# Kernel tuning notes

Measured on AMD Instinct MI355X. Metric: run time of the kernel, lower is better.

## Reference

```python
import jax, jax.numpy as jnp
import numpy as np

B, CQ, CK, H, W = 8, 256, 256, 96, 96
EPS = 1e-4
SLOPE = 0.01  # torch LeakyReLU default


def conv1x1(x, w, b):
    # x: [B,Ci,H,W], w: [Co,Ci], b: [Co]
    return jnp.einsum('oi,bihw->bohw', w, x) + b[None, :, None, None]


def setup_inputs() -> dict:
    key = jax.random.key(0)
    ks = jax.random.split(key, 8)
    s = 0.02  # weight init scale for numerical sanity
    return {
        'q': jax.random.normal(ks[0], (B, CQ, H, W), jnp.float32),
        'v': jax.random.normal(ks[1], (B, CK, H, W), jnp.float32),
        'Wq': jax.random.normal(ks[2], (CQ, CQ), jnp.float32) * s,
        'bq': jnp.zeros((CQ,), jnp.float32),
        'Wk': jax.random.normal(ks[3], (CK, CK), jnp.float32) * s,
        'bk': jnp.zeros((CK,), jnp.float32),
        'Wv': jax.random.normal(ks[4], (CK, CQ), jnp.float32) * s,
        'bv': jnp.zeros((CK,), jnp.float32),
        'bn_gamma': jnp.ones((CQ,), jnp.float32),
        'bn_beta': jnp.zeros((CQ,), jnp.float32),
        'bn_mean': jnp.zeros((CQ,), jnp.float32),
        'bn_var': jnp.ones((CQ,), jnp.float32),
        'Wo1': jax.random.normal(ks[5], (CQ, CQ), jnp.float32) * s,
        'bo1': jnp.zeros((CQ,), jnp.float32),
        'Wo2': jax.random.normal(ks[6], (CQ, CQ), jnp.float32) * s,
        'bo2': jnp.zeros((CQ,), jnp.float32),
    }


def reference(q, v, Wq, bq, Wk, bk, Wv, bv, bn_gamma, bn_beta, bn_mean, bn_var, Wo1, bo1, Wo2, bo2):
    N = H * W
    query = conv1x1(q, Wq, bq).reshape(B, CQ, N)   # [B,CQ,N]
    key_t = conv1x1(v, Wk, bk).reshape(B, CK, N)   # [B,CK,N]
    value = conv1x1(q, Wv, bv).reshape(B, CK, N)   # [B,CK,N]
    # channel-attention: scores over channels, spatial is the contraction axis
    scale = float(N) ** 0.5
    scores = jnp.einsum('bcn,bdn->bcd', query, key_t) / scale  # [B,CQ,CK]
    attn = jax.nn.softmax(scores, axis=-1)
    out = jnp.einsum('bcd,bdn->bcn', attn, value)  # [B,CQ,N]
    # faithful permute(0,2,1).contiguous().view(B,-1,H,W): raw reshape of [B,N,CQ]
    out = jnp.transpose(out, (0, 2, 1)).reshape(B, CQ, H, W)
    # conv_out: BN (inference) -> LeakyReLU -> 1x1 conv -> LeakyReLU -> 1x1 conv
    inv = jax.lax.rsqrt(bn_var + EPS)
    out = (out - bn_mean[None, :, None, None]) * (bn_gamma * inv)[None, :, None, None] + bn_beta[None, :, None, None]
    out = jnp.where(out >= 0, out, SLOPE * out)
    out = conv1x1(out, Wo1, bo1)
    out = jnp.where(out >= 0, out, SLOPE * out)
    out = conv1x1(out, Wo2, bo2)
    return out
```

## Files before the change

### kernel.cpp

```cpp
#include <hip/hip_runtime.h>
#include <hip/hip_bf16.h>
#include <stdint.h>

#define CH     256
#define NSP    9216
#define NBATCH 8
#define NSPLIT 8
#define KSEG   1152

typedef unsigned short ushort_t;
using f32x4  = __attribute__((ext_vector_type(4))) float;
using bf16x8 = __attribute__((ext_vector_type(8))) short;

__device__ __forceinline__ ushort_t f2b(float f) {
  union { float f; uint32_t u; } v; v.f = f;
  return (ushort_t)((v.u + 0x7FFFu + ((v.u >> 16) & 1u)) >> 16);
}

__device__ __forceinline__ uint32_t swz(uint32_t row, uint32_t byte) {
  return row * 128u + (byte ^ ((row & 7u) << 4));
}

typedef __attribute__((address_space(3))) void       lds_void;
typedef const __attribute__((address_space(1))) void g_void;
__device__ __forceinline__ void glds16(const void* g, void* l) {
  __builtin_amdgcn_global_load_lds((g_void*)g, (lds_void*)l, 16, 0, 0);
}

__global__ void wconv_kernel(const float* __restrict__ w0, const float* __restrict__ w1,
                             const float* __restrict__ w2, const float* __restrict__ w3,
                             const float* __restrict__ w4, ushort_t* __restrict__ dst) {
  int gid = blockIdx.x * 256 + threadIdx.x;
  int m   = gid >> 13;
  int u   = gid & 8191;
  const float* W = (m == 0) ? w0 : (m == 1) ? w1 : (m == 2) ? w2 : (m == 3) ? w3 : w4;
  int lin = u * 16;
  int kc  = lin >> 15;
  int co  = (lin >> 7) & 255;
  int bb0 = lin & 127;
  int k0  = kc * 64 + ((bb0 ^ ((co & 7) << 4)) >> 1);
  const float* srow = W + co * 256 + k0;
  float4 a = *reinterpret_cast<const float4*>(srow);
  float4 c = *reinterpret_cast<const float4*>(srow + 4);
  ushort_t o[8] = {f2b(a.x), f2b(a.y), f2b(a.z), f2b(a.w),
                   f2b(c.x), f2b(c.y), f2b(c.z), f2b(c.w)};
  uint4 pk;
  pk.x = (uint32_t)o[0] | ((uint32_t)o[1] << 16);
  pk.y = (uint32_t)o[2] | ((uint32_t)o[3] << 16);
  pk.z = (uint32_t)o[4] | ((uint32_t)o[5] << 16);
  pk.w = (uint32_t)o[6] | ((uint32_t)o[7] << 16);
  *reinterpret_cast<uint4*>(dst + m * 65536 + (lin >> 1)) = pk;
}

template<int NOUT>
__global__ __launch_bounds__(256)
void proj_kernel(const ushort_t* __restrict__ Asw0, const float* __restrict__ bias0,
                 ushort_t* __restrict__ dst0,
                 const ushort_t* __restrict__ Asw1, const float* __restrict__ bias1,
                 char* __restrict__ valt,
                 const float* __restrict__ src) {
  const int b    = blockIdx.y;
  const int n0   = blockIdx.x * 64;
  const int tid  = threadIdx.x;
  const int lane = tid & 63;
  const int w    = tid >> 6;

  __shared__ __align__(16) unsigned char sA0[32768];
  __shared__ __align__(16) unsigned char sA1[(NOUT == 2) ? 32768 : 16];
  __shared__ __align__(16) unsigned char sB[8192];

  f32x4 acc0[4][4];
  f32x4 acc1[4][4];
  #pragma unroll
  for (int i = 0; i < 4; ++i)
    #pragma unroll
    for (int j = 0; j < 4; ++j)
      #pragma unroll
      for (int r = 0; r < 4; ++r) { acc0[i][j][r] = 0.f; acc1[i][j][r] = 0.f; }

  for (int kc = 0; kc < 4; ++kc) {
    const int k0 = kc * 64;
    if (kc > 0) __syncthreads();
    #pragma unroll
    for (int it = 0; it < 8; ++it) {
      int seg = (it * 4 + w) * 1024;
      glds16((const char*)Asw0 + kc * 32768 + seg + lane * 16,
             (void*)(sA0 + seg));
      if constexpr (NOUT == 2)
        glds16((const char*)Asw1 + kc * 32768 + seg + lane * 16,
               (void*)(sA1 + seg));
    }
    {
      const int ci0 = (tid >> 4) * 4;
      const int n4  = (tid & 15) * 4;
      float xv[4][4];
      #pragma unroll
      for (int r = 0; r < 4; ++r) {
        float4 t4 = *reinterpret_cast<const float4*>(
            src + ((size_t)b * CH + (k0 + ci0 + r)) * NSP + n0 + n4);
        xv[r][0] = t4.x; xv[r][1] = t4.y; xv[r][2] = t4.z; xv[r][3] = t4.w;
      }
      #pragma unroll
      for (int j = 0; j < 4; ++j) {
        uint64_t pk = (uint64_t)f2b(xv[0][j])
                    | ((uint64_t)f2b(xv[1][j]) << 16)
                    | ((uint64_t)f2b(xv[2][j]) << 32)
                    | ((uint64_t)f2b(xv[3][j]) << 48);
        *reinterpret_cast<uint64_t*>(&sB[swz(n4 + j, ci0 * 2)]) = pk;
      }
    }
    __syncthreads();
    #pragma unroll
    for (int ks = 0; ks < 2; ++ks) {
      const int kb = ks * 64 + (lane >> 4) * 16;
      bf16x8 fb[4], fa0[4];
      #pragma unroll
      for (int ni = 0; ni < 4; ++ni)
        fb[ni] = *reinterpret_cast<const bf16x8*>(&sB[swz(ni * 16 + (lane & 15), kb)]);
      #pragma unroll
      for (int mi = 0; mi < 4; ++mi)
        fa0[mi] = *reinterpret_cast<const bf16x8*>(&sA0[swz(w * 64 + mi * 16 + (lane & 15), kb)]);
      #pragma unroll
      for (int mi = 0; mi < 4; ++mi)
        #pragma unroll
        for (int ni = 0; ni < 4; ++ni)
          acc0[mi][ni] = __builtin_amdgcn_mfma_f32_16x16x32_bf16(fa0[mi], fb[ni], acc0[mi][ni], 0, 0, 0);
      if constexpr (NOUT == 2) {
        bf16x8 fa1[4];
        #pragma unroll
        for (int mi = 0; mi < 4; ++mi)
          fa1[mi] = *reinterpret_cast<const bf16x8*>(&sA1[swz(w * 64 + mi * 16 + (lane & 15), kb)]);
        #pragma unroll
        for (int mi = 0; mi < 4; ++mi)
          #pragma unroll
          for (int ni = 0; ni < 4; ++ni)
            acc1[mi][ni] = __builtin_amdgcn_mfma_f32_16x16x32_bf16(fa1[mi], fb[ni], acc1[mi][ni], 0, 0, 0);
      }
    }
  }
  #pragma unroll
  for (int mi = 0; mi < 4; ++mi) {
    const int coB = w * 64 + mi * 16 + ((lane >> 4) << 2);
    #pragma unroll
    for (int ni = 0; ni < 4; ++ni) {
      const int n = n0 + ni * 16 + (lane & 15);
      #pragma unroll
      for (int r = 0; r < 4; ++r) {
        const int co = coB + r;
        dst0[((size_t)b * CH + co) * NSP + n] = f2b(acc0[mi][ni][r] + bias0[co]);
      }
    }
  }
  if constexpr (NOUT == 2) {
    __syncthreads();
    #pragma unroll
    for (int mi = 0; mi < 4; ++mi) {
      const int co0 = w * 64 + mi * 16 + ((lane >> 4) << 2);
      #pragma unroll
      for (int ni = 0; ni < 4; ++ni) {
        const int nl = ni * 16 + (lane & 15);
        uint64_t pk = (uint64_t)f2b(acc1[mi][ni][0] + bias1[co0])
                    | ((uint64_t)f2b(acc1[mi][ni][1] + bias1[co0 + 1]) << 16)
                    | ((uint64_t)f2b(acc1[mi][ni][2] + bias1[co0 + 2]) << 32)
                    | ((uint64_t)f2b(acc1[mi][ni][3] + bias1[co0 + 3]) << 48);
        *reinterpret_cast<uint64_t*>(&sA0[nl * 512 + ((co0 * 2) ^ ((nl & 7) << 4))]) = pk;
      }
    }
    __syncthreads();
    char* vb = valt + (size_t)b * (NSP * 512) + (size_t)n0 * 512;
    #pragma unroll
    for (int i = 0; i < 8; ++i) {
      *reinterpret_cast<uint4*>(vb + tid * 128 + i * 16) =
          *reinterpret_cast<const uint4*>(sA0 + tid * 128 + i * 16);
    }
  }
}

__global__ __launch_bounds__(256)
void scores_kernel(const ushort_t* __restrict__ qry, const ushort_t* __restrict__ key,
                   float* __restrict__ part) {
  const int b  = blockIdx.z;
  const int s  = blockIdx.y;
  const int c0 = (blockIdx.x >> 1) * 128;
  const int d0 = (blockIdx.x & 1) * 128;
  const int tid  = threadIdx.x;
  const int lane = tid & 63;
  const int wm = (tid >> 7) & 1;
  const int wn = (tid >> 6) & 1;

  __shared__ __align__(16) unsigned char sQ[128 * 128];
  __shared__ __align__(16) unsigned char sK[128 * 128];

  f32x4 acc[4][4];
  #pragma unroll
  for (int i = 0; i < 4; ++i)
    #pragma unroll
    for (int j = 0; j < 4; ++j)
      #pragma unroll
      for (int r = 0; r < 4; ++r) acc[i][j][r] = 0.f;

  for (int kc = 0; kc < KSEG / 64; ++kc) {
    const int k0 = s * KSEG + kc * 64;
    #pragma unroll
    for (int it = 0; it < 4; ++it) {
      int slot = it * 256 + tid;
      int row  = slot >> 3;
      int seg  = slot & 7;
      *reinterpret_cast<uint4*>(&sQ[swz(row, seg * 16)]) =
          *reinterpret_cast<const uint4*>(qry + ((size_t)b * CH + c0 + row) * NSP + k0 + seg * 8);
      *reinterpret_cast<uint4*>(&sK[swz(row, seg * 16)]) =
          *reinterpret_cast<const uint4*>(key + ((size_t)b * CH + d0 + row) * NSP + k0 + seg * 8);
    }
    __syncthreads();
    #pragma unroll
    for (int ks = 0; ks < 2; ++ks) {
      const int kb = ks * 64 + (lane >> 4) * 16;
      bf16x8 fq[4], fk[4];
      #pragma unroll
      for (int mi = 0; mi < 4; ++mi)
        fq[mi] = *reinterpret_cast<const bf16x8*>(&sQ[swz(wm * 64 + mi * 16 + (lane & 15), kb)]);
      #pragma unroll
      for (int ni = 0; ni < 4; ++ni)
        fk[ni] = *reinterpret_cast<const bf16x8*>(&sK[swz(wn * 64 + ni * 16 + (lane & 15), kb)]);
      #pragma unroll
      for (int mi = 0; mi < 4; ++mi)
        #pragma unroll
        for (int ni = 0; ni < 4; ++ni)
          acc[mi][ni] = __builtin_amdgcn_mfma_f32_16x16x32_bf16(fq[mi], fk[ni], acc[mi][ni], 0, 0, 0);
    }
    __syncthreads();
  }
  const size_t base = ((size_t)b * NSPLIT + s) * CH;
  #pragma unroll
  for (int mi = 0; mi < 4; ++mi) {
    #pragma unroll
    for (int ni = 0; ni < 4; ++ni) {
      #pragma unroll
      for (int r = 0; r < 4; ++r) {
        int c = c0 + wm * 64 + mi * 16 + ((lane >> 4) << 2) + r;
        int d = d0 + wn * 64 + ni * 16 + (lane & 15);
        part[(base + c) * CH + d] = acc[mi][ni][r];
      }
    }
  }
}

__global__ __launch_bounds__(64)
void softmax_kernel(const float* __restrict__ part, ushort_t* __restrict__ attn) {
  const int c = blockIdx.x;
  const int b = blockIdx.y;
  const int lane = threadIdx.x;
  float sv[4] = {0.f, 0.f, 0.f, 0.f};
  for (int sp = 0; sp < NSPLIT; ++sp) {
    const float* p = part + (((size_t)b * NSPLIT + sp) * CH + c) * CH;
    #pragma unroll
    for (int r = 0; r < 4; ++r) sv[r] += p[r * 64 + lane];
  }
  #pragma unroll
  for (int r = 0; r < 4; ++r) sv[r] *= (1.0f / 96.0f);
  float m = fmaxf(fmaxf(sv[0], sv[1]), fmaxf(sv[2], sv[3]));
  for (int off = 32; off > 0; off >>= 1) m = fmaxf(m, __shfl_xor(m, off));
  float e[4]; float sum = 0.f;
  #pragma unroll
  for (int r = 0; r < 4; ++r) { e[r] = expf(sv[r] - m); sum += e[r]; }
  for (int off = 32; off > 0; off >>= 1) sum += __shfl_xor(sum, off);
  float inv = 1.0f / sum;
  ushort_t* ap = attn + ((size_t)b * CH + c) * CH;
  #pragma unroll
  for (int r = 0; r < 4; ++r) ap[r * 64 + lane] = f2b(e[r] * inv);
}

__global__ __launch_bounds__(512)
void mega_kernel(const ushort_t* __restrict__ attn, const char* __restrict__ valt,
                 const ushort_t* __restrict__ w1sw, const float* __restrict__ bo1,
                 const ushort_t* __restrict__ w2sw, const float* __restrict__ bo2,
                 const float* __restrict__ gamma, const float* __restrict__ beta,
                 const float* __restrict__ mean,  const float* __restrict__ var,
                 float* __restrict__ out) {
  const int b    = blockIdx.y;
  const int s    = blockIdx.x >> 2;
  const int c0   = (blockIdx.x & 3) * 64;
  const int tid  = threadIdx.x;
  const int lane = tid & 63;
  const int w    = tid >> 6;

  __shared__ __align__(16) unsigned char L[104 * 1024];
  unsigned char* sS = L;
  unsigned char* sV = L + 8192;
  unsigned char* sT = L + 40960;
  unsigned char* sW = L + 73728;
  unsigned char* sO = L;

  const ushort_t* attn_b = attn + (size_t)b * 65536;
  const char*     vt_b   = valt + (size_t)b * (NSP * 512);

  f32x4 acc[4][2];
  #pragma unroll
  for (int i = 0; i < 4; ++i)
    #pragma unroll
    for (int j = 0; j < 2; ++j)
      #pragma unroll
      for (int r = 0; r < 4; ++r) acc[i][j][r] = 0.f;

  for (int kc = 0; kc < 4; ++kc) {
    if (kc > 0) __syncthreads();
    {
      int row = tid >> 3, seg = tid & 7;
      *reinterpret_cast<uint4*>(&sS[swz(row, seg * 16)]) =
          *reinterpret_cast<const uint4*>(attn_b + (c0 + row) * 256 + kc * 64 + seg * 8);
    }
    #pragma unroll
    for (int it = 0; it < 4; ++it) {
      int slot = it * 512 + tid;
      int j = slot >> 3, seg = slot & 7;
      int n = s + 36 * j;
      uint4 dv = *reinterpret_cast<const uint4*>(
          vt_b + n * 512 + ((kc * 128 + seg * 16) ^ ((n & 7) << 4)));
      *reinterpret_cast<uint4*>(&sV[swz(j, seg * 16)]) = dv;
    }
    __syncthreads();
    #pragma unroll
    for (int ks = 0; ks < 2; ++ks) {
      const int kb = ks * 64 + (lane >> 4) * 16;
      bf16x8 fa[4], fb[2];
      #pragma unroll
      for (int mi = 0; mi < 4; ++mi)
        fa[mi] = *reinterpret_cast<const bf16x8*>(&sS[swz(mi * 16 + (lane & 15), kb)]);
      #pragma unroll
      for (int ni = 0; ni < 2; ++ni)
        fb[ni] = *reinterpret_cast<const bf16x8*>(&sV[swz(w * 32 + ni * 16 + (lane & 15), kb)]);
      #pragma unroll
      for (int mi = 0; mi < 4; ++mi)
        #pragma unroll
        for (int ni = 0; ni < 2; ++ni)
          acc[mi][ni] = __builtin_amdgcn_mfma_f32_16x16x32_bf16(fa[mi], fb[ni], acc[mi][ni], 0, 0, 0);
    }
  }
  {
    float kf[2], bb[2];
    #pragma unroll
    for (int ni = 0; ni < 2; ++ni) {
      int j = w * 32 + ni * 16 + (lane & 15);
      float iv = rsqrtf(var[j] + 1e-4f);
      kf[ni] = gamma[j] * iv;
      bb[ni] = beta[j] - mean[j] * kf[ni];
    }
    #pragma unroll
    for (int mi = 0; mi < 4; ++mi)
      #pragma unroll
      for (int ni = 0; ni < 2; ++ni) {
        int j = w * 32 + ni * 16 + (lane & 15);
        #pragma unroll
        for (int r = 0; r < 4; ++r) {
          int cl = mi * 16 + ((lane >> 4) << 2) + r;
          float x = acc[mi][ni][r] * kf[ni] + bb[ni];
          x = (x >= 0.f) ? x : 0.01f * x;
          *reinterpret_cast<ushort_t*>(&sT[cl * 512 + ((j * 2) ^ ((cl & 7) << 4))]) = f2b(x);
        }
      }
  }
  __syncthreads();

  f32x4 a2[2][4];
  #pragma unroll
  for (int i = 0; i < 2; ++i)
    #pragma unroll
    for (int j = 0; j < 4; ++j)
      #pragma unroll
      for (int r = 0; r < 4; ++r) a2[i][j][r] = 0.f;

  for (int kc = 0; kc < 4; ++kc) {
    if (kc > 0) __syncthreads();
    #pragma unroll
    for (int it = 0; it < 4; ++it) {
      int seg = (it * 8 + w) * 1024;
      glds16((const char*)w1sw + kc * 32768 + seg + lane * 16, (void*)(sW + seg));
    }
    __syncthreads();
    #pragma unroll
    for (int ks = 0; ks < 2; ++ks) {
      const int kbw = ks * 64 + (lane >> 4) * 16;
      const int kbt = kc * 128 + kbw;
      bf16x8 fa2[2], fb2[4];
      #pragma unroll
      for (int mi = 0; mi < 2; ++mi)
        fa2[mi] = *reinterpret_cast<const bf16x8*>(&sW[swz(w * 32 + mi * 16 + (lane & 15), kbw)]);
      #pragma unroll
      for (int ni = 0; ni < 4; ++ni) {
        int cl = ni * 16 + (lane & 15);
        fb2[ni] = *reinterpret_cast<const bf16x8*>(&sT[cl * 512 + (kbt ^ ((cl & 7) << 4))]);
      }
      #pragma unroll
      for (int mi = 0; mi < 2; ++mi)
        #pragma unroll
        for (int ni = 0; ni < 4; ++ni)
          a2[mi][ni] = __builtin_amdgcn_mfma_f32_16x16x32_bf16(fa2[mi], fb2[ni], a2[mi][ni], 0, 0, 0);
    }
  }
  #pragma unroll
  for (int mi = 0; mi < 2; ++mi) {
    const int co0 = w * 32 + mi * 16 + ((lane >> 4) << 2);
    #pragma unroll
    for (int ni = 0; ni < 4; ++ni) {
      const int cl = ni * 16 + (lane & 15);
      float y[4];
      #pragma unroll
      for (int r = 0; r < 4; ++r) {
        y[r] = a2[mi][ni][r] + bo1[co0 + r];
        y[r] = (y[r] >= 0.f) ? y[r] : 0.01f * y[r];
      }
      uint64_t pk = (uint64_t)f2b(y[0]) | ((uint64_t)f2b(y[1]) << 16)
                  | ((uint64_t)f2b(y[2]) << 32) | ((uint64_t)f2b(y[3]) << 48);
      *reinterpret_cast<uint64_t*>(&sO[cl * 512 + ((co0 * 2) ^ ((cl & 7) << 4))]) = pk;
    }
  }
  __syncthreads();

  f32x4 a3[2][4];
  #pragma unroll
  for (int i = 0; i < 2; ++i)
    #pragma unroll
    for (int j = 0; j < 4; ++j)
      #pragma unroll
      for (int r = 0; r < 4; ++r) a3[i][j][r] = 0.f;

  for (int kc = 0; kc < 4; ++kc) {
    if (kc > 0) __syncthreads();
    #pragma unroll
    for (int it = 0; it < 4; ++it) {
      int seg = (it * 8 + w) * 1024;
      glds16((const char*)w2sw + kc * 32768 + seg + lane * 16, (void*)(sW + seg));
    }
    __syncthreads();
    #pragma unroll
    for (int ks = 0; ks < 2; ++ks) {
      const int kbw = ks * 64 + (lane >> 4) * 16;
      const int kbt = kc * 128 + kbw;
      bf16x8 fa3[2], fb3[4];
      #pragma unroll
      for (int mi = 0; mi < 2; ++mi)
        fa3[mi] = *reinterpret_cast<const bf16x8*>(&sW[swz(w * 32 + mi * 16 + (lane & 15), kbw)]);
      #pragma unroll
      for (int ni = 0; ni < 4; ++ni) {
        int cl = ni * 16 + (lane & 15);
        fb3[ni] = *reinterpret_cast<const bf16x8*>(&sO[cl * 512 + (kbt ^ ((cl & 7) << 4))]);
      }
      #pragma unroll
      for (int mi = 0; mi < 2; ++mi)
        #pragma unroll
        for (int ni = 0; ni < 4; ++ni)
          a3[mi][ni] = __builtin_amdgcn_mfma_f32_16x16x32_bf16(fa3[mi], fb3[ni], a3[mi][ni], 0, 0, 0);
    }
  }
  #pragma unroll
  for (int mi = 0; mi < 2; ++mi) {
    const int coB = w * 32 + mi * 16 + ((lane >> 4) << 2);
    #pragma unroll
    for (int ni = 0; ni < 4; ++ni) {
      const int cl = ni * 16 + (lane & 15);
      #pragma unroll
      for (int r = 0; r < 4; ++r) {
        const int co = coB + r;
        out[(size_t)b * (CH * NSP) + (size_t)co * NSP + s * 256 + c0 + cl] =
            a3[mi][ni][r] + bo2[co];
      }
    }
  }
}

extern "C" void kernel_launch(void* const* d_in, const int* in_sizes, int n_in,
                              void* d_out, int out_size, void* d_ws, size_t ws_size,
                              hipStream_t stream) {
  (void)in_sizes; (void)n_in; (void)out_size; (void)ws_size;
  const float* q   = (const float*)d_in[0];
  const float* v   = (const float*)d_in[1];
  const float* Wq  = (const float*)d_in[2];
  const float* bq  = (const float*)d_in[3];
  const float* Wk  = (const float*)d_in[4];
  const float* bk  = (const float*)d_in[5];
  const float* Wv  = (const float*)d_in[6];
  const float* bv  = (const float*)d_in[7];
  const float* bng = (const float*)d_in[8];
  const float* bnb = (const float*)d_in[9];
  const float* bnm = (const float*)d_in[10];
  const float* bnv = (const float*)d_in[11];
  const float* Wo1 = (const float*)d_in[12];
  const float* bo1 = (const float*)d_in[13];
  const float* Wo2 = (const float*)d_in[14];
  const float* bo2 = (const float*)d_in[15];

  char* ws = (char*)d_ws;
  ushort_t* wq_b  = (ushort_t*)(ws);
  ushort_t* wk_b  = (ushort_t*)(ws + 131072);
  ushort_t* wv_b  = (ushort_t*)(ws + 262144);
  ushort_t* wo1_b = (ushort_t*)(ws + 393216);
  ushort_t* wo2_b = (ushort_t*)(ws + 524288);
  char*     valt  = ws + 655360;
  float*    part  = (float*)   (ws + 655360 + 37748736);
  ushort_t* attn  = (ushort_t*)(ws + 655360 + 37748736 + 16777216);
  ushort_t* qry   = (ushort_t*)d_out;
  ushort_t* key   = qry + 18874368;

  wconv_kernel<<<160, 256, 0, stream>>>(Wq, Wk, Wv, Wo1, Wo2, wq_b);

  dim3 g1(NSP / 64, NBATCH);
  proj_kernel<2><<<g1, 256, 0, stream>>>(wq_b, bq, qry, wv_b, bv, valt, q);
  proj_kernel<1><<<g1, 256, 0, stream>>>(wk_b, bk, key, nullptr, nullptr, nullptr, v);

  scores_kernel<<<dim3(4, NSPLIT, NBATCH), 256, 0, stream>>>(qry, key, part);
  softmax_kernel<<<dim3(CH, NBATCH), 64, 0, stream>>>(part, attn);

  mega_kernel<<<dim3(144, NBATCH), 512, 0, stream>>>(
      attn, valt, wo1_b, bo1, wo2_b, bo2, bng, bnb, bnm, bnv, (float*)d_out);
}
```

Measured before the change: 403.2 us.

## Read output-conv weights directly from global memory and remap blocks across XCDs

The two output 1x1-conv GEMMs in the fused kernel now read their bf16 weight fragments straight from global memory in a plain row-major layout (the weight converter skips the swizzle for those matrices). This removes the per-chunk LDS staging and its barriers, and cuts shared memory from 104 KB to 72 KB, which may allow more blocks per CU. Block indices are also permuted so consecutive hardware block IDs map to different batches, likely to spread L2 locality across XCDs. The cost is uncoalesced-ish global/L2 reads of weights repeated by every block instead of one shared LDS copy.

```diff
diff --git a/kernel.cpp b/kernel.cpp
--- a/kernel.cpp
+++ b/kernel.cpp
@@ -35,11 +35,16 @@
   int u   = gid & 8191;
   const float* W = (m == 0) ? w0 : (m == 1) ? w1 : (m == 2) ? w2 : (m == 3) ? w3 : w4;
   int lin = u * 16;
-  int kc  = lin >> 15;
-  int co  = (lin >> 7) & 255;
-  int bb0 = lin & 127;
-  int k0  = kc * 64 + ((bb0 ^ ((co & 7) << 4)) >> 1);
-  const float* srow = W + co * 256 + k0;
+  const float* srow;
+  if (m < 3) {
+    int kc  = lin >> 15;
+    int co  = (lin >> 7) & 255;
+    int bb0 = lin & 127;
+    int k0  = kc * 64 + ((bb0 ^ ((co & 7) << 4)) >> 1);
+    srow = W + co * 256 + k0;
+  } else {
+    srow = W + u * 8;
+  }
   float4 a = *reinterpret_cast<const float4*>(srow);
   float4 c = *reinterpret_cast<const float4*>(srow + 4);
   ushort_t o[8] = {f2b(a.x), f2b(a.y), f2b(a.z), f2b(a.w),
@@ -272,23 +277,25 @@
 
 __global__ __launch_bounds__(512)
 void mega_kernel(const ushort_t* __restrict__ attn, const char* __restrict__ valt,
-                 const ushort_t* __restrict__ w1sw, const float* __restrict__ bo1,
-                 const ushort_t* __restrict__ w2sw, const float* __restrict__ bo2,
+                 const ushort_t* __restrict__ w1p, const float* __restrict__ bo1,
+                 const ushort_t* __restrict__ w2p, const float* __restrict__ bo2,
                  const float* __restrict__ gamma, const float* __restrict__ beta,
                  const float* __restrict__ mean,  const float* __restrict__ var,
                  float* __restrict__ out) {
-  const int b    = blockIdx.y;
-  const int s    = blockIdx.x >> 2;
-  const int c0   = (blockIdx.x & 3) * 64;
+  const int lin = blockIdx.y * 144 + blockIdx.x;
+  const int wid = (lin & 7) * 144 + (lin >> 3);
+  const int b   = wid / 144;
+  const int rr  = wid % 144;
+  const int s   = rr >> 2;
+  const int c0  = (rr & 3) * 64;
   const int tid  = threadIdx.x;
   const int lane = tid & 63;
   const int w    = tid >> 6;
 
-  __shared__ __align__(16) unsigned char L[104 * 1024];
+  __shared__ __align__(16) unsigned char L[72 * 1024];
   unsigned char* sS = L;
   unsigned char* sV = L + 8192;
   unsigned char* sT = L + 40960;
-  unsigned char* sW = L + 73728;
   unsigned char* sO = L;
 
   const ushort_t* attn_b = attn + (size_t)b * 65536;
@@ -369,22 +376,17 @@
       #pragma unroll
       for (int r = 0; r < 4; ++r) a2[i][j][r] = 0.f;
 
+  #pragma unroll
   for (int kc = 0; kc < 4; ++kc) {
-    if (kc > 0) __syncthreads();
-    #pragma unroll
-    for (int it = 0; it < 4; ++it) {
-      int seg = (it * 8 + w) * 1024;
-      glds16((const char*)w1sw + kc * 32768 + seg + lane * 16, (void*)(sW + seg));
-    }
-    __syncthreads();
     #pragma unroll
     for (int ks = 0; ks < 2; ++ks) {
-      const int kbw = ks * 64 + (lane >> 4) * 16;
-      const int kbt = kc * 128 + kbw;
+      const int ke  = kc * 64 + ks * 32 + (lane >> 4) * 8;
+      const int kbt = kc * 128 + ks * 64 + (lane >> 4) * 16;
       bf16x8 fa2[2], fb2[4];
       #pragma unroll
       for (int mi = 0; mi < 2; ++mi)
-        fa2[mi] = *reinterpret_cast<const bf16x8*>(&sW[swz(w * 32 + mi * 16 + (lane & 15), kbw)]);
+        fa2[mi] = *reinterpret_cast<const bf16x8*>(
+            w1p + (w * 32 + mi * 16 + (lane & 15)) * 256 + ke);
       #pragma unroll
       for (int ni = 0; ni < 4; ++ni) {
         int cl = ni * 16 + (lane & 15);
@@ -424,22 +426,17 @@
       #pragma unroll
       for (int r = 0; r < 4; ++r) a3[i][j][r] = 0.f;
 
+  #pragma unroll
   for (int kc = 0; kc < 4; ++kc) {
-    if (kc > 0) __syncthreads();
-    #pragma unroll
-    for (int it = 0; it < 4; ++it) {
-      int seg = (it * 8 + w) * 1024;
-      glds16((const char*)w2sw + kc * 32768 + seg + lane * 16, (void*)(sW + seg));
-    }
-    __syncthreads();
     #pragma unroll
     for (int ks = 0; ks < 2; ++ks) {
-      const int kbw = ks * 64 + (lane >> 4) * 16;
-      const int kbt = kc * 128 + kbw;
+      const int ke  = kc * 64 + ks * 32 + (lane >> 4) * 8;
+      const int kbt = kc * 128 + ks * 64 + (lane >> 4) * 16;
       bf16x8 fa3[2], fb3[4];
       #pragma unroll
       for (int mi = 0; mi < 2; ++mi)
-        fa3[mi] = *reinterpret_cast<const bf16x8*>(&sW[swz(w * 32 + mi * 16 + (lane & 15), kbw)]);
+        fa3[mi] = *reinterpret_cast<const bf16x8*>(
+            w2p + (w * 32 + mi * 16 + (lane & 15)) * 256 + ke);
       #pragma unroll
       for (int ni = 0; ni < 4; ++ni) {
         int cl = ni * 16 + (lane & 15);
```

Result: faster. 380.2 us (-5.7%).
